# Optimization experiments

Measured on AMD Instinct MI355X. Metric: run time of the kernel, lower is better.

## Reference

```python
import jax, jax.numpy as jnp
import numpy as np

B, N, C, H = 128, 8732, 512, 19  # batch, priors, channels, feature map side
IMG = 300.0
FG = 19


def setup_inputs() -> dict:
    key = jax.random.key(0)
    ks = jax.random.split(key, 10)
    loc = jax.random.normal(ks[0], (B, N, 4), jnp.float32) * 0.5
    conf = jax.random.normal(ks[1], (B, N, 2), jnp.float32)
    priors = jax.random.uniform(ks[2], (N, 4), jnp.float32, minval=0.05, maxval=0.95)
    features = jax.random.normal(ks[3], (B, C, H, H), jnp.float32)
    w1 = jax.random.normal(ks[4], (C, 4096), jnp.float32) * 0.01
    b1 = jnp.zeros((4096,), jnp.float32)
    w2 = jax.random.normal(ks[5], (4096, 4096), jnp.float32) * 0.01
    b2 = jnp.zeros((4096,), jnp.float32)
    w3 = jax.random.normal(ks[6], (4096, FG), jnp.float32) * 0.01
    b3 = jnp.zeros((FG,), jnp.float32)
    return {"loc": loc, "conf": conf, "priors": priors, "features": features,
            "w1": w1, "b1": b1, "w2": w2, "b2": b2, "w3": w3, "b3": b3}


def _decode(loc, priors):
    # SSD decode, variances=[0.1, 0.2]; priors are (cx, cy, w, h)
    cxcy = priors[:, :2] + loc[..., :2] * 0.1 * priors[:, 2:]
    wh = priors[:, 2:] * jnp.exp(loc[..., 2:] * 0.2)
    xy1 = cxcy - 0.5 * wh
    return jnp.concatenate([xy1, xy1 + wh], axis=-1)  # [B,N,4] corner form


def _best_prior(loc, conf, priors):
    boxes = _decode(loc, priors)                       # [B,N,4]
    probs = jax.nn.softmax(conf, axis=-1)              # [B,N,2]
    car = jnp.argmax(probs, axis=-1) == 1              # [B,N] argmax class == car
    score = jnp.where(car, probs[..., 1], -jnp.inf)
    best = jnp.argmax(score, axis=-1)                  # [B]
    best_box = jnp.take_along_axis(boxes, best[:, None, None], axis=1)[:, 0]  # [B,4]
    has_car = jnp.any(car, axis=-1)                    # [B]
    geom = (best_box[:, 2] > best_box[:, 0]) & (best_box[:, 3] > best_box[:, 1])
    valid = has_car & geom
    result = jnp.where(has_car[:, None], best_box, 0.0)
    result = jnp.clip(result, 0.0, 1.0)
    return result, valid


def _extract(features, boxes, valid):
    # per-box crop + global max pool -> [B,C], zero for invalid boxes
    ceil_num = features.shape[2]
    step = IMG / ceil_num
    b = jnp.clip(boxes * IMG, 0.0, IMG) / step
    b = jnp.floor(jnp.clip(b, 0.0, ceil_num - 1.0)).astype(jnp.int32)  # [B,4]=x1,y1,x2,y2
    r = jnp.arange(ceil_num)
    mh = (r[None, :] >= b[:, 1:2]) & (r[None, :] <= b[:, 3:4])  # [B,H] rows
    mw = (r[None, :] >= b[:, 0:1]) & (r[None, :] <= b[:, 2:3])  # [B,W] cols
    mask = mh[:, None, :, None] & mw[:, None, None, :]          # [B,1,H,W]
    m = jnp.max(jnp.where(mask, features, -jnp.inf), axis=(2, 3))  # [B,C]
    return jnp.where(valid[:, None], m, 0.0)


def reference(loc, conf, priors, features, w1, b1, w2, b2, w3, b3):
    boxes, valid = _best_prior(loc, conf, priors)
    feat = _extract(features, boxes, valid)             # [B,512]
    h = jax.nn.relu(feat @ w1 + b1)
    h = jax.nn.relu(h @ w2 + b2)
    fg_cls = h @ w3 + b3                                # [B,19]
    return fg_cls, boxes, valid.astype(jnp.int32)
```

## Files before the change

kernel.cpp:

```cpp
#include <hip/hip_runtime.h>
#include <hip/hip_bf16.h>
#include <math.h>

#define BATCH 128
#define NPRI  8732
#define CCH   512
#define HH    19
#define NHID  4096
#define FGC   19

typedef unsigned short u16;
typedef __attribute__((ext_vector_type(8))) short bf16x8;
typedef __attribute__((ext_vector_type(4))) float f32x4;

__device__ __forceinline__ u16 f2bf(float f) {
  unsigned u = __float_as_uint(f);
  u += 0x7fff + ((u >> 16) & 1);
  return (u16)(u >> 16);
}

__global__ void k_best_partial(const float* __restrict__ conf,
                               float* __restrict__ cs, int* __restrict__ ci,
                               int* __restrict__ cc) {
  int blk = blockIdx.x;
  int b = blk >> 2, chunk = blk & 3;
  int n0 = chunk * 2183;
  int t = threadIdx.x;
  const float* cb = conf + (size_t)b * NPRI * 2;
  float bestS = -INFINITY; int bestN = 0x7fffffff; int car_any = 0;
  for (int i = n0 + t; i < n0 + 2183; i += 256) {
    float c0 = cb[2 * i], c1 = cb[2 * i + 1];
    float m = fmaxf(c0, c1);
    float e0 = expf(c0 - m), e1 = expf(c1 - m);
    float s = e0 + e1;
    float p0 = e0 / s, p1 = e1 / s;
    bool car = p1 > p0;
    car_any |= (int)car;
    float sc = car ? p1 : -INFINITY;
    if (sc > bestS || (sc == bestS && i < bestN)) { bestS = sc; bestN = i; }
  }
  __shared__ float ls[256]; __shared__ int li[256]; __shared__ int lc[256];
  ls[t] = bestS; li[t] = bestN; lc[t] = car_any;
  __syncthreads();
  for (int off = 128; off > 0; off >>= 1) {
    if (t < off) {
      float s2 = ls[t + off]; int n2 = li[t + off];
      if (s2 > ls[t] || (s2 == ls[t] && n2 < li[t])) { ls[t] = s2; li[t] = n2; }
      lc[t] |= lc[t + off];
    }
    __syncthreads();
  }
  if (t == 0) { cs[blk] = ls[0]; ci[blk] = li[0]; cc[blk] = lc[0]; }
}

__global__ void k_best_final(const float* __restrict__ loc,
                             const float* __restrict__ priors,
                             const float* __restrict__ cs,
                             const int* __restrict__ ci,
                             const int* __restrict__ cc,
                             float* __restrict__ out_boxes,
                             float* __restrict__ out_valid,
                             int4* __restrict__ crop,
                             int* __restrict__ vflag) {
  int b = threadIdx.x;
  if (b >= BATCH) return;
  float bs = -INFINITY; int bn = 0; int hc = 0;
  #pragma unroll
  for (int p = 0; p < 4; p++) {
    float s = cs[b * 4 + p]; int n = ci[b * 4 + p];
    hc |= cc[b * 4 + p];
    if (s > bs) { bs = s; bn = n; }
  }
  const float* lp = loc + ((size_t)b * NPRI + bn) * 4;
  const float* pp = priors + (size_t)bn * 4;
  float l0 = lp[0], l1 = lp[1], l2 = lp[2], l3 = lp[3];
  float pcx = pp[0], pcy = pp[1], pw = pp[2], ph = pp[3];
  float cx = pcx + (l0 * 0.1f) * pw;
  float cy = pcy + (l1 * 0.1f) * ph;
  float w = pw * expf(l2 * 0.2f);
  float h = ph * expf(l3 * 0.2f);
  float x1 = cx - 0.5f * w;
  float y1 = cy - 0.5f * h;
  float x2 = x1 + w, y2 = y1 + h;
  bool geom = (x2 > x1) && (y2 > y1);
  bool valid = hc && geom;
  float r0, r1, r2, r3;
  if (hc) { r0 = x1; r1 = y1; r2 = x2; r3 = y2; }
  else    { r0 = r1 = r2 = r3 = 0.0f; }
  r0 = fminf(fmaxf(r0, 0.0f), 1.0f);
  r1 = fminf(fmaxf(r1, 0.0f), 1.0f);
  r2 = fminf(fmaxf(r2, 0.0f), 1.0f);
  r3 = fminf(fmaxf(r3, 0.0f), 1.0f);
  out_boxes[b * 4 + 0] = r0; out_boxes[b * 4 + 1] = r1;
  out_boxes[b * 4 + 2] = r2; out_boxes[b * 4 + 3] = r3;
  out_valid[b] = valid ? 1.0f : 0.0f;
  const float stepF = (float)(300.0 / 19.0);
  float q0 = fminf(fmaxf(r0 * 300.0f, 0.0f), 300.0f) / stepF;
  float q1 = fminf(fmaxf(r1 * 300.0f, 0.0f), 300.0f) / stepF;
  float q2 = fminf(fmaxf(r2 * 300.0f, 0.0f), 300.0f) / stepF;
  float q3 = fminf(fmaxf(r3 * 300.0f, 0.0f), 300.0f) / stepF;
  int ix1 = (int)floorf(fminf(fmaxf(q0, 0.0f), 18.0f));
  int iy1 = (int)floorf(fminf(fmaxf(q1, 0.0f), 18.0f));
  int ix2 = (int)floorf(fminf(fmaxf(q2, 0.0f), 18.0f));
  int iy2 = (int)floorf(fminf(fmaxf(q3, 0.0f), 18.0f));
  crop[b] = make_int4(ix1, iy1, ix2, iy2);
  vflag[b] = valid ? 1 : 0;
}

__global__ void k_extract(const float* __restrict__ fin,
                          const int4* __restrict__ crop,
                          const int* __restrict__ vflag,
                          u16* __restrict__ feat) {
  int blk = blockIdx.x;
  int b = blk >> 7;
  int tile = blk & 127;
  int wave = threadIdx.x >> 6;
  int lane = threadIdx.x & 63;
  int c = tile * 4 + wave;
  if (!vflag[b]) {
    if (lane == 0) feat[b * CCH + c] = 0;
    return;
  }
  int4 cr = crop[b];
  int wcnt = cr.z - cr.x + 1;
  int cnt = wcnt * (cr.w - cr.y + 1);
  const float* p = fin + (size_t)(b * CCH + c) * (HH * HH);
  float m = -INFINITY;
  for (int i = lane; i < cnt; i += 64) {
    int yy = cr.y + i / wcnt;
    int xx = cr.x + i % wcnt;
    m = fmaxf(m, p[yy * HH + xx]);
  }
  #pragma unroll
  for (int off = 32; off > 0; off >>= 1) m = fmaxf(m, __shfl_xor(m, off));
  if (lane == 0) feat[b * CCH + c] = f2bf(m);
}

template <int KSPL>
__global__ __launch_bounds__(256) void k_mfma(const u16* __restrict__ A,
                                              const float* __restrict__ W,
                                              float* __restrict__ part, int K) {
  const int N = 4096;
  const int BK = 32;
  int nb = blockIdx.x;
  int ks = blockIdx.y;
  int Kper = K / KSPL;
  int k0b = ks * Kper;
  int t = threadIdx.x;
  int lane = t & 63, wave = t >> 6;
  int q = lane >> 4, r = lane & 15;

  __shared__ u16 As[128 * 40];
  __shared__ u16 Bs[64 * 40];

  int wm = (wave & 1) * 64;
  int wn = (wave >> 1) * 32;
  int n0 = nb * 64;

  f32x4 acc[4][2];
  #pragma unroll
  for (int i = 0; i < 4; i++)
    #pragma unroll
    for (int j = 0; j < 2; j++) {
      acc[i][j].x = 0.f; acc[i][j].y = 0.f; acc[i][j].z = 0.f; acc[i][j].w = 0.f;
    }

  int am = t >> 1, ah = (t & 1) * 16;
  int kp = t >> 4;
  int n4 = (t & 15) * 4;

  for (int k0 = k0b; k0 < k0b + Kper; k0 += BK) {
    const u16* asrc = A + (size_t)am * K + k0 + ah;
    uint4 a0 = *(const uint4*)asrc;
    uint4 a1 = *(const uint4*)(asrc + 8);
    const float* wsrc = W + (size_t)(k0 + 2 * kp) * N + n0 + n4;
    float4 w0 = *(const float4*)wsrc;
    float4 w1 = *(const float4*)(wsrc + N);
    __syncthreads();
    *(uint4*)&As[am * 40 + ah]     = a0;
    *(uint4*)&As[am * 40 + ah + 8] = a1;
    {
      unsigned pk0 = (unsigned)f2bf(w0.x) | ((unsigned)f2bf(w1.x) << 16);
      unsigned pk1 = (unsigned)f2bf(w0.y) | ((unsigned)f2bf(w1.y) << 16);
      unsigned pk2 = (unsigned)f2bf(w0.z) | ((unsigned)f2bf(w1.z) << 16);
      unsigned pk3 = (unsigned)f2bf(w0.w) | ((unsigned)f2bf(w1.w) << 16);
      *(unsigned*)&Bs[(n4 + 0) * 40 + 2 * kp] = pk0;
      *(unsigned*)&Bs[(n4 + 1) * 40 + 2 * kp] = pk1;
      *(unsigned*)&Bs[(n4 + 2) * 40 + 2 * kp] = pk2;
      *(unsigned*)&Bs[(n4 + 3) * 40 + 2 * kp] = pk3;
    }
    __syncthreads();
    bf16x8 af[4], bfr[2];
    #pragma unroll
    for (int i = 0; i < 4; i++)
      af[i] = *(const bf16x8*)&As[(wm + 16 * i + r) * 40 + q * 8];
    #pragma unroll
    for (int j = 0; j < 2; j++)
      bfr[j] = *(const bf16x8*)&Bs[(wn + 16 * j + r) * 40 + q * 8];
    #pragma unroll
    for (int i = 0; i < 4; i++)
      #pragma unroll
      for (int j = 0; j < 2; j++)
        acc[i][j] = __builtin_amdgcn_mfma_f32_16x16x32_bf16(af[i], bfr[j],
                                                            acc[i][j], 0, 0, 0);
  }

  float* dst = part + (size_t)ks * (BATCH * N);
  #pragma unroll
  for (int i = 0; i < 4; i++)
    #pragma unroll
    for (int j = 0; j < 2; j++) {
      int col = n0 + wn + 16 * j + r;
      #pragma unroll
      for (int reg = 0; reg < 4; reg++) {
        int row = wm + 16 * i + q * 4 + reg;
        dst[(size_t)row * N + col] = acc[i][j][reg];
      }
    }
}

template <int KSPL, bool BF16OUT>
__global__ void k_finalize(const float* __restrict__ part,
                           const float* __restrict__ bias,
                           float* __restrict__ outf,
                           u16* __restrict__ outb) {
  int idx = (blockIdx.x * 256 + threadIdx.x) * 4;
  float4 s = *(const float4*)(part + idx);
  #pragma unroll
  for (int p = 1; p < KSPL; p++) {
    float4 v = *(const float4*)(part + (size_t)p * (BATCH * NHID) + idx);
    s.x += v.x; s.y += v.y; s.z += v.z; s.w += v.w;
  }
  float4 bv = *(const float4*)(bias + (idx & (NHID - 1)));
  s.x = fmaxf(s.x + bv.x, 0.0f); s.y = fmaxf(s.y + bv.y, 0.0f);
  s.z = fmaxf(s.z + bv.z, 0.0f); s.w = fmaxf(s.w + bv.w, 0.0f);
  if (BF16OUT) {
    ushort4 o;
    o.x = f2bf(s.x); o.y = f2bf(s.y); o.z = f2bf(s.z); o.w = f2bf(s.w);
    *(ushort4*)(outb + idx) = o;
  } else {
    *(float4*)(outf + idx) = s;
  }
}

__global__ void k_gemm3p(const float* __restrict__ h2,
                         const float* __restrict__ w3,
                         float* __restrict__ part3) {
  int kc = blockIdx.x;
  int t = threadIdx.x;
  __shared__ float wl[32 * FGC];
  for (int i = t; i < 32 * FGC; i += 128) wl[i] = w3[kc * 32 * FGC + i];
  __syncthreads();
  const float* hp = h2 + (size_t)t * NHID + kc * 32;
  float acc[FGC];
  #pragma unroll
  for (int j = 0; j < FGC; j++) acc[j] = 0.0f;
  for (int k = 0; k < 32; k++) {
    float hv = hp[k];
    const float* wp = &wl[k * FGC];
    #pragma unroll
    for (int j = 0; j < FGC; j++) acc[j] += hv * wp[j];
  }
  float* dst = part3 + (size_t)kc * (BATCH * FGC) + t * FGC;
  #pragma unroll
  for (int j = 0; j < FGC; j++) dst[j] = acc[j];
}

__global__ void k_fin3(const float* __restrict__ part3,
                       const float* __restrict__ b3,
                       float* __restrict__ out) {
  int j = blockIdx.x * 256 + threadIdx.x;
  if (j >= BATCH * FGC) return;
  float s = 0.0f;
  for (int p = 0; p < 128; p++) s += part3[(size_t)p * (BATCH * FGC) + j];
  out[j] = s + b3[j % FGC];
}

extern "C" void kernel_launch(void* const* d_in, const int* in_sizes, int n_in,
                              void* d_out, int out_size, void* d_ws, size_t ws_size,
                              hipStream_t stream) {
  const float* loc      = (const float*)d_in[0];
  const float* conf     = (const float*)d_in[1];
  const float* priors   = (const float*)d_in[2];
  const float* features = (const float*)d_in[3];
  const float* w1 = (const float*)d_in[4];
  const float* b1 = (const float*)d_in[5];
  const float* w2 = (const float*)d_in[6];
  const float* b2 = (const float*)d_in[7];
  const float* w3 = (const float*)d_in[8];
  const float* b3 = (const float*)d_in[9];
  float* out = (float*)d_out;

  char* ws = (char*)d_ws;
  float* part  = (float*)ws;
  float* part3 = (float*)(ws + (size_t)16 * 1024 * 1024);
  float* h2    = (float*)(ws + (size_t)18 * 1024 * 1024);
  u16*   featb = (u16*)(ws + (size_t)20 * 1024 * 1024);
  u16*   h1b   = (u16*)(ws + (size_t)20 * 1024 * 1024 + 256 * 1024);
  float* cs    = (float*)(ws + (size_t)21 * 1024 * 1024);
  int*   ci    = (int*)(cs + 512);
  int*   cc    = ci + 512;
  int4*  crop  = (int4*)(cc + 512);
  int*   vfl   = (int*)(crop + BATCH);

  k_best_partial<<<512, 256, 0, stream>>>(conf, cs, ci, cc);
  k_best_final<<<1, 128, 0, stream>>>(loc, priors, cs, ci, cc,
                                      out + BATCH * FGC,
                                      out + BATCH * FGC + BATCH * 4, crop, vfl);
  k_extract<<<BATCH * (CCH / 4), 256, 0, stream>>>(features, crop, vfl, featb);
  k_mfma<4><<<dim3(64, 4), 256, 0, stream>>>(featb, w1, part, 512);
  k_finalize<4, true><<<512, 256, 0, stream>>>(part, b1, nullptr, h1b);
  k_mfma<8><<<dim3(64, 8), 256, 0, stream>>>(h1b, w2, part, 4096);
  k_finalize<8, false><<<512, 256, 0, stream>>>(part, b2, h2, nullptr);
  k_gemm3p<<<128, 128, 0, stream>>>(h2, w3, part3);
  k_fin3<<<10, 256, 0, stream>>>(part3, b3, out);
}
```

Measured before the change: 260.6 us.

## Fuse whole pipeline into one cooperative persistent kernel with grid syncs

Replaces nine separate kernel launches with one cooperative kernel of 512 blocks that runs every stage in sequence, separated by grid-wide barriers. The best-prior search now uses one block per batch row and compares logit differences instead of computing softmax. The first GEMM now uses a K split of 8 instead of 4, and the final 19-wide projection becomes one block per row with shuffle reductions. The aim is to remove per-launch overhead and intermediate round trips, at the cost of grid-sync latency and fewer blocks in the extract and final-projection stages.

```diff
diff --git a/kernel.cpp b/kernel.cpp
--- a/kernel.cpp
+++ b/kernel.cpp
@@ -1,6 +1,8 @@
 #include <hip/hip_runtime.h>
-#include <hip/hip_bf16.h>
+#include <hip/hip_cooperative_groups.h>
 #include <math.h>
+
+namespace cg = cooperative_groups;
 
 #define BATCH 128
 #define NPRI  8732
@@ -8,6 +10,8 @@
 #define HH    19
 #define NHID  4096
 #define FGC   19
+#define GRID  512
+#define KSPL  8
 
 typedef unsigned short u16;
 typedef __attribute__((ext_vector_type(8))) short bf16x8;
@@ -19,142 +23,25 @@
   return (u16)(u >> 16);
 }
 
-__global__ void k_best_partial(const float* __restrict__ conf,
-                               float* __restrict__ cs, int* __restrict__ ci,
-                               int* __restrict__ cc) {
-  int blk = blockIdx.x;
-  int b = blk >> 2, chunk = blk & 3;
-  int n0 = chunk * 2183;
-  int t = threadIdx.x;
-  const float* cb = conf + (size_t)b * NPRI * 2;
-  float bestS = -INFINITY; int bestN = 0x7fffffff; int car_any = 0;
-  for (int i = n0 + t; i < n0 + 2183; i += 256) {
-    float c0 = cb[2 * i], c1 = cb[2 * i + 1];
-    float m = fmaxf(c0, c1);
-    float e0 = expf(c0 - m), e1 = expf(c1 - m);
-    float s = e0 + e1;
-    float p0 = e0 / s, p1 = e1 / s;
-    bool car = p1 > p0;
-    car_any |= (int)car;
-    float sc = car ? p1 : -INFINITY;
-    if (sc > bestS || (sc == bestS && i < bestN)) { bestS = sc; bestN = i; }
-  }
-  __shared__ float ls[256]; __shared__ int li[256]; __shared__ int lc[256];
-  ls[t] = bestS; li[t] = bestN; lc[t] = car_any;
-  __syncthreads();
-  for (int off = 128; off > 0; off >>= 1) {
-    if (t < off) {
-      float s2 = ls[t + off]; int n2 = li[t + off];
-      if (s2 > ls[t] || (s2 == ls[t] && n2 < li[t])) { ls[t] = s2; li[t] = n2; }
-      lc[t] |= lc[t + off];
-    }
-    __syncthreads();
-  }
-  if (t == 0) { cs[blk] = ls[0]; ci[blk] = li[0]; cc[blk] = lc[0]; }
-}
-
-__global__ void k_best_final(const float* __restrict__ loc,
-                             const float* __restrict__ priors,
-                             const float* __restrict__ cs,
-                             const int* __restrict__ ci,
-                             const int* __restrict__ cc,
-                             float* __restrict__ out_boxes,
-                             float* __restrict__ out_valid,
-                             int4* __restrict__ crop,
-                             int* __restrict__ vflag) {
-  int b = threadIdx.x;
-  if (b >= BATCH) return;
-  float bs = -INFINITY; int bn = 0; int hc = 0;
-  #pragma unroll
-  for (int p = 0; p < 4; p++) {
-    float s = cs[b * 4 + p]; int n = ci[b * 4 + p];
-    hc |= cc[b * 4 + p];
-    if (s > bs) { bs = s; bn = n; }
-  }
-  const float* lp = loc + ((size_t)b * NPRI + bn) * 4;
-  const float* pp = priors + (size_t)bn * 4;
-  float l0 = lp[0], l1 = lp[1], l2 = lp[2], l3 = lp[3];
-  float pcx = pp[0], pcy = pp[1], pw = pp[2], ph = pp[3];
-  float cx = pcx + (l0 * 0.1f) * pw;
-  float cy = pcy + (l1 * 0.1f) * ph;
-  float w = pw * expf(l2 * 0.2f);
-  float h = ph * expf(l3 * 0.2f);
-  float x1 = cx - 0.5f * w;
-  float y1 = cy - 0.5f * h;
-  float x2 = x1 + w, y2 = y1 + h;
-  bool geom = (x2 > x1) && (y2 > y1);
-  bool valid = hc && geom;
-  float r0, r1, r2, r3;
-  if (hc) { r0 = x1; r1 = y1; r2 = x2; r3 = y2; }
-  else    { r0 = r1 = r2 = r3 = 0.0f; }
-  r0 = fminf(fmaxf(r0, 0.0f), 1.0f);
-  r1 = fminf(fmaxf(r1, 0.0f), 1.0f);
-  r2 = fminf(fmaxf(r2, 0.0f), 1.0f);
-  r3 = fminf(fmaxf(r3, 0.0f), 1.0f);
-  out_boxes[b * 4 + 0] = r0; out_boxes[b * 4 + 1] = r1;
-  out_boxes[b * 4 + 2] = r2; out_boxes[b * 4 + 3] = r3;
-  out_valid[b] = valid ? 1.0f : 0.0f;
-  const float stepF = (float)(300.0 / 19.0);
-  float q0 = fminf(fmaxf(r0 * 300.0f, 0.0f), 300.0f) / stepF;
-  float q1 = fminf(fmaxf(r1 * 300.0f, 0.0f), 300.0f) / stepF;
-  float q2 = fminf(fmaxf(r2 * 300.0f, 0.0f), 300.0f) / stepF;
-  float q3 = fminf(fmaxf(r3 * 300.0f, 0.0f), 300.0f) / stepF;
-  int ix1 = (int)floorf(fminf(fmaxf(q0, 0.0f), 18.0f));
-  int iy1 = (int)floorf(fminf(fmaxf(q1, 0.0f), 18.0f));
-  int ix2 = (int)floorf(fminf(fmaxf(q2, 0.0f), 18.0f));
-  int iy2 = (int)floorf(fminf(fmaxf(q3, 0.0f), 18.0f));
-  crop[b] = make_int4(ix1, iy1, ix2, iy2);
-  vflag[b] = valid ? 1 : 0;
-}
-
-__global__ void k_extract(const float* __restrict__ fin,
-                          const int4* __restrict__ crop,
-                          const int* __restrict__ vflag,
-                          u16* __restrict__ feat) {
-  int blk = blockIdx.x;
-  int b = blk >> 7;
-  int tile = blk & 127;
-  int wave = threadIdx.x >> 6;
-  int lane = threadIdx.x & 63;
-  int c = tile * 4 + wave;
-  if (!vflag[b]) {
-    if (lane == 0) feat[b * CCH + c] = 0;
-    return;
-  }
-  int4 cr = crop[b];
-  int wcnt = cr.z - cr.x + 1;
-  int cnt = wcnt * (cr.w - cr.y + 1);
-  const float* p = fin + (size_t)(b * CCH + c) * (HH * HH);
-  float m = -INFINITY;
-  for (int i = lane; i < cnt; i += 64) {
-    int yy = cr.y + i / wcnt;
-    int xx = cr.x + i % wcnt;
-    m = fmaxf(m, p[yy * HH + xx]);
-  }
-  #pragma unroll
-  for (int off = 32; off > 0; off >>= 1) m = fmaxf(m, __shfl_xor(m, off));
-  if (lane == 0) feat[b * CCH + c] = f2bf(m);
-}
-
-template <int KSPL>
-__global__ __launch_bounds__(256) void k_mfma(const u16* __restrict__ A,
-                                              const float* __restrict__ W,
-                                              float* __restrict__ part, int K) {
-  const int N = 4096;
-  const int BK = 32;
-  int nb = blockIdx.x;
-  int ks = blockIdx.y;
-  int Kper = K / KSPL;
+struct SMem {
+  union {
+    struct { float s[256]; int n[256]; } red;
+    struct { u16 As[128 * 40]; u16 Bs[64 * 40]; } mm;
+    float g3[4 * FGC];
+  };
+};
+
+__device__ void mfma_phase(const u16* __restrict__ A, const float* __restrict__ W,
+                           float* __restrict__ part, int K, int Kper,
+                           u16* As, u16* Bs) {
+  const int N = NHID;
+  int bid = blockIdx.x;
+  int nb = bid & 63, ks = bid >> 6;
   int k0b = ks * Kper;
   int t = threadIdx.x;
   int lane = t & 63, wave = t >> 6;
   int q = lane >> 4, r = lane & 15;
-
-  __shared__ u16 As[128 * 40];
-  __shared__ u16 Bs[64 * 40];
-
-  int wm = (wave & 1) * 64;
-  int wn = (wave >> 1) * 32;
+  int wm = (wave & 1) * 64, wn = (wave >> 1) * 32;
   int n0 = nb * 64;
 
   f32x4 acc[4][2];
@@ -169,21 +56,21 @@
   int kp = t >> 4;
   int n4 = (t & 15) * 4;
 
-  for (int k0 = k0b; k0 < k0b + Kper; k0 += BK) {
+  for (int k0 = k0b; k0 < k0b + Kper; k0 += 32) {
     const u16* asrc = A + (size_t)am * K + k0 + ah;
     uint4 a0 = *(const uint4*)asrc;
     uint4 a1 = *(const uint4*)(asrc + 8);
     const float* wsrc = W + (size_t)(k0 + 2 * kp) * N + n0 + n4;
     float4 w0 = *(const float4*)wsrc;
-    float4 w1 = *(const float4*)(wsrc + N);
+    float4 w1v = *(const float4*)(wsrc + N);
     __syncthreads();
     *(uint4*)&As[am * 40 + ah]     = a0;
     *(uint4*)&As[am * 40 + ah + 8] = a1;
     {
-      unsigned pk0 = (unsigned)f2bf(w0.x) | ((unsigned)f2bf(w1.x) << 16);
-      unsigned pk1 = (unsigned)f2bf(w0.y) | ((unsigned)f2bf(w1.y) << 16);
-      unsigned pk2 = (unsigned)f2bf(w0.z) | ((unsigned)f2bf(w1.z) << 16);
-      unsigned pk3 = (unsigned)f2bf(w0.w) | ((unsigned)f2bf(w1.w) << 16);
+      unsigned pk0 = (unsigned)f2bf(w0.x) | ((unsigned)f2bf(w1v.x) << 16);
+      unsigned pk1 = (unsigned)f2bf(w0.y) | ((unsigned)f2bf(w1v.y) << 16);
+      unsigned pk2 = (unsigned)f2bf(w0.z) | ((unsigned)f2bf(w1v.z) << 16);
+      unsigned pk3 = (unsigned)f2bf(w0.w) | ((unsigned)f2bf(w1v.w) << 16);
       *(unsigned*)&Bs[(n4 + 0) * 40 + 2 * kp] = pk0;
       *(unsigned*)&Bs[(n4 + 1) * 40 + 2 * kp] = pk1;
       *(unsigned*)&Bs[(n4 + 2) * 40 + 2 * kp] = pk2;
@@ -205,7 +92,7 @@
                                                             acc[i][j], 0, 0, 0);
   }
 
-  float* dst = part + (size_t)ks * (BATCH * N);
+  float* dst = part + (size_t)ks * (BATCH * NHID);
   #pragma unroll
   for (int i = 0; i < 4; i++)
     #pragma unroll
@@ -219,61 +106,171 @@
     }
 }
 
-template <int KSPL, bool BF16OUT>
-__global__ void k_finalize(const float* __restrict__ part,
-                           const float* __restrict__ bias,
-                           float* __restrict__ outf,
-                           u16* __restrict__ outb) {
-  int idx = (blockIdx.x * 256 + threadIdx.x) * 4;
-  float4 s = *(const float4*)(part + idx);
-  #pragma unroll
-  for (int p = 1; p < KSPL; p++) {
-    float4 v = *(const float4*)(part + (size_t)p * (BATCH * NHID) + idx);
-    s.x += v.x; s.y += v.y; s.z += v.z; s.w += v.w;
-  }
-  float4 bv = *(const float4*)(bias + (idx & (NHID - 1)));
-  s.x = fmaxf(s.x + bv.x, 0.0f); s.y = fmaxf(s.y + bv.y, 0.0f);
-  s.z = fmaxf(s.z + bv.z, 0.0f); s.w = fmaxf(s.w + bv.w, 0.0f);
-  if (BF16OUT) {
+__global__ __launch_bounds__(256, 2) void fused_net(
+    const float* __restrict__ loc, const float* __restrict__ conf,
+    const float* __restrict__ priors, const float* __restrict__ features,
+    const float* __restrict__ w1, const float* __restrict__ b1,
+    const float* __restrict__ w2, const float* __restrict__ b2,
+    const float* __restrict__ w3, const float* __restrict__ b3,
+    float* __restrict__ out, float* __restrict__ part,
+    u16* __restrict__ featb, u16* __restrict__ h1b, float* __restrict__ h2,
+    int4* __restrict__ crop, int* __restrict__ vfl) {
+  __shared__ __align__(16) SMem sm;
+  cg::grid_group grid = cg::this_grid();
+  int t = threadIdx.x;
+
+  if (blockIdx.x < BATCH) {
+    int b = blockIdx.x;
+    const float4* cb = (const float4*)(conf + (size_t)b * NPRI * 2);
+    float bd = -INFINITY; int bn = 0x7fffffff;
+    for (int j = t; j < NPRI / 2; j += 256) {
+      float4 v = cb[j];
+      float d0 = v.y - v.x, d1 = v.w - v.z;
+      if (d0 > bd) { bd = d0; bn = 2 * j; }
+      if (d1 > bd) { bd = d1; bn = 2 * j + 1; }
+    }
+    sm.red.s[t] = bd; sm.red.n[t] = bn;
+    __syncthreads();
+    for (int off = 128; off > 0; off >>= 1) {
+      if (t < off) {
+        float s2 = sm.red.s[t + off]; int n2 = sm.red.n[t + off];
+        if (s2 > sm.red.s[t] || (s2 == sm.red.s[t] && n2 < sm.red.n[t])) {
+          sm.red.s[t] = s2; sm.red.n[t] = n2;
+        }
+      }
+      __syncthreads();
+    }
+    if (t == 0) {
+      float bdf = sm.red.s[0]; int bnf = sm.red.n[0];
+      bool hc = bdf > 0.0f;
+      float r0 = 0.f, r1 = 0.f, r2 = 0.f, r3 = 0.f;
+      bool valid = false;
+      if (hc) {
+        const float* lp = loc + ((size_t)b * NPRI + bnf) * 4;
+        const float* pp = priors + (size_t)bnf * 4;
+        float l0 = lp[0], l1 = lp[1], l2 = lp[2], l3 = lp[3];
+        float pcx = pp[0], pcy = pp[1], pw = pp[2], ph = pp[3];
+        float cx = pcx + (l0 * 0.1f) * pw;
+        float cy = pcy + (l1 * 0.1f) * ph;
+        float w = pw * expf(l2 * 0.2f);
+        float h = ph * expf(l3 * 0.2f);
+        float x1 = cx - 0.5f * w, y1 = cy - 0.5f * h;
+        float x2 = x1 + w, y2 = y1 + h;
+        valid = (x2 > x1) && (y2 > y1);
+        r0 = fminf(fmaxf(x1, 0.f), 1.f);
+        r1 = fminf(fmaxf(y1, 0.f), 1.f);
+        r2 = fminf(fmaxf(x2, 0.f), 1.f);
+        r3 = fminf(fmaxf(y2, 0.f), 1.f);
+      }
+      float* ob = out + BATCH * FGC;
+      ob[b * 4 + 0] = r0; ob[b * 4 + 1] = r1;
+      ob[b * 4 + 2] = r2; ob[b * 4 + 3] = r3;
+      out[BATCH * FGC + BATCH * 4 + b] = valid ? 1.0f : 0.0f;
+      const float stepF = (float)(300.0 / 19.0);
+      float q0 = fminf(fmaxf(r0 * 300.0f, 0.0f), 300.0f) / stepF;
+      float q1 = fminf(fmaxf(r1 * 300.0f, 0.0f), 300.0f) / stepF;
+      float q2 = fminf(fmaxf(r2 * 300.0f, 0.0f), 300.0f) / stepF;
+      float q3 = fminf(fmaxf(r3 * 300.0f, 0.0f), 300.0f) / stepF;
+      int ix1 = (int)floorf(fminf(fmaxf(q0, 0.0f), 18.0f));
+      int iy1 = (int)floorf(fminf(fmaxf(q1, 0.0f), 18.0f));
+      int ix2 = (int)floorf(fminf(fmaxf(q2, 0.0f), 18.0f));
+      int iy2 = (int)floorf(fminf(fmaxf(q3, 0.0f), 18.0f));
+      crop[b] = make_int4(ix1, iy1, ix2, iy2);
+      vfl[b] = valid ? 1 : 0;
+    }
+  }
+  grid.sync();
+
+  {
+    int wave = t >> 6, lane = t & 63;
+    for (int v = blockIdx.x; v < BATCH * (CCH / 4); v += GRID) {
+      int b = v >> 7, tile = v & 127;
+      int c = tile * 4 + wave;
+      if (!vfl[b]) { if (lane == 0) featb[b * CCH + c] = 0; continue; }
+      int4 cr = crop[b];
+      int wcnt = cr.z - cr.x + 1;
+      int cnt = wcnt * (cr.w - cr.y + 1);
+      const float* p = features + (size_t)(b * CCH + c) * (HH * HH);
+      float m = -INFINITY;
+      for (int i = lane; i < cnt; i += 64) {
+        int yy = cr.y + i / wcnt;
+        int xx = cr.x + i % wcnt;
+        m = fmaxf(m, p[yy * HH + xx]);
+      }
+      #pragma unroll
+      for (int off = 32; off > 0; off >>= 1) m = fmaxf(m, __shfl_xor(m, off));
+      if (lane == 0) featb[b * CCH + c] = f2bf(m);
+    }
+  }
+  grid.sync();
+
+  mfma_phase(featb, w1, part, CCH, CCH / KSPL, sm.mm.As, sm.mm.Bs);
+  grid.sync();
+
+  {
+    int idx = (blockIdx.x * 256 + t) * 4;
+    float4 s = *(const float4*)(part + idx);
+    #pragma unroll
+    for (int p = 1; p < KSPL; p++) {
+      float4 v = *(const float4*)(part + (size_t)p * (BATCH * NHID) + idx);
+      s.x += v.x; s.y += v.y; s.z += v.z; s.w += v.w;
+    }
+    float4 bv = *(const float4*)(b1 + (idx & (NHID - 1)));
+    s.x = fmaxf(s.x + bv.x, 0.0f); s.y = fmaxf(s.y + bv.y, 0.0f);
+    s.z = fmaxf(s.z + bv.z, 0.0f); s.w = fmaxf(s.w + bv.w, 0.0f);
     ushort4 o;
     o.x = f2bf(s.x); o.y = f2bf(s.y); o.z = f2bf(s.z); o.w = f2bf(s.w);
-    *(ushort4*)(outb + idx) = o;
-  } else {
-    *(float4*)(outf + idx) = s;
-  }
-}
-
-__global__ void k_gemm3p(const float* __restrict__ h2,
-                         const float* __restrict__ w3,
-                         float* __restrict__ part3) {
-  int kc = blockIdx.x;
-  int t = threadIdx.x;
-  __shared__ float wl[32 * FGC];
-  for (int i = t; i < 32 * FGC; i += 128) wl[i] = w3[kc * 32 * FGC + i];
-  __syncthreads();
-  const float* hp = h2 + (size_t)t * NHID + kc * 32;
-  float acc[FGC];
-  #pragma unroll
-  for (int j = 0; j < FGC; j++) acc[j] = 0.0f;
-  for (int k = 0; k < 32; k++) {
-    float hv = hp[k];
-    const float* wp = &wl[k * FGC];
-    #pragma unroll
-    for (int j = 0; j < FGC; j++) acc[j] += hv * wp[j];
-  }
-  float* dst = part3 + (size_t)kc * (BATCH * FGC) + t * FGC;
-  #pragma unroll
-  for (int j = 0; j < FGC; j++) dst[j] = acc[j];
-}
-
-__global__ void k_fin3(const float* __restrict__ part3,
-                       const float* __restrict__ b3,
-                       float* __restrict__ out) {
-  int j = blockIdx.x * 256 + threadIdx.x;
-  if (j >= BATCH * FGC) return;
-  float s = 0.0f;
-  for (int p = 0; p < 128; p++) s += part3[(size_t)p * (BATCH * FGC) + j];
-  out[j] = s + b3[j % FGC];
+    *(ushort4*)(h1b + idx) = o;
+  }
+  grid.sync();
+
+  mfma_phase(h1b, w2, part, NHID, NHID / KSPL, sm.mm.As, sm.mm.Bs);
+  grid.sync();
+
+  {
+    int idx = (blockIdx.x * 256 + t) * 4;
+    float4 s = *(const float4*)(part + idx);
+    #pragma unroll
+    for (int p = 1; p < KSPL; p++) {
+      float4 v = *(const float4*)(part + (size_t)p * (BATCH * NHID) + idx);
+      s.x += v.x; s.y += v.y; s.z += v.z; s.w += v.w;
+    }
+    float4 bv = *(const float4*)(b2 + (idx & (NHID - 1)));
+    s.x = fmaxf(s.x + bv.x, 0.0f); s.y = fmaxf(s.y + bv.y, 0.0f);
+    s.z = fmaxf(s.z + bv.z, 0.0f); s.w = fmaxf(s.w + bv.w, 0.0f);
+    *(float4*)(h2 + idx) = s;
+  }
+  grid.sync();
+
+  if (blockIdx.x < BATCH) {
+    int b = blockIdx.x;
+    float acc[FGC];
+    #pragma unroll
+    for (int j = 0; j < FGC; j++) acc[j] = 0.0f;
+    const float* hp = h2 + (size_t)b * NHID;
+    for (int k = t; k < NHID; k += 256) {
+      float hv = hp[k];
+      const float* wp = w3 + (size_t)k * FGC;
+      #pragma unroll
+      for (int j = 0; j < FGC; j++) acc[j] += hv * wp[j];
+    }
+    int lane = t & 63, wave = t >> 6;
+    #pragma unroll
+    for (int j = 0; j < FGC; j++) {
+      #pragma unroll
+      for (int off = 32; off > 0; off >>= 1)
+        acc[j] += __shfl_xor(acc[j], off);
+    }
+    if (lane == 0) {
+      #pragma unroll
+      for (int j = 0; j < FGC; j++) sm.g3[wave * FGC + j] = acc[j];
+    }
+    __syncthreads();
+    if (t < FGC) {
+      float s = sm.g3[t] + sm.g3[FGC + t] + sm.g3[2 * FGC + t] + sm.g3[3 * FGC + t];
+      out[b * FGC + t] = s + b3[t];
+    }
+  }
 }
 
 extern "C" void kernel_launch(void* const* d_in, const int* in_sizes, int n_in,
@@ -293,25 +290,18 @@
 
   char* ws = (char*)d_ws;
   float* part  = (float*)ws;
-  float* part3 = (float*)(ws + (size_t)16 * 1024 * 1024);
+  u16*   featb = (u16*)(ws + (size_t)16 * 1024 * 1024);
+  u16*   h1b   = (u16*)(ws + (size_t)16 * 1024 * 1024 + 256 * 1024);
   float* h2    = (float*)(ws + (size_t)18 * 1024 * 1024);
-  u16*   featb = (u16*)(ws + (size_t)20 * 1024 * 1024);
-  u16*   h1b   = (u16*)(ws + (size_t)20 * 1024 * 1024 + 256 * 1024);
-  float* cs    = (float*)(ws + (size_t)21 * 1024 * 1024);
-  int*   ci    = (int*)(cs + 512);
-  int*   cc    = ci + 512;
-  int4*  crop  = (int4*)(cc + 512);
+  int4*  crop  = (int4*)(ws + (size_t)20 * 1024 * 1024);
   int*   vfl   = (int*)(crop + BATCH);
 
-  k_best_partial<<<512, 256, 0, stream>>>(conf, cs, ci, cc);
-  k_best_final<<<1, 128, 0, stream>>>(loc, priors, cs, ci, cc,
-                                      out + BATCH * FGC,
-                                      out + BATCH * FGC + BATCH * 4, crop, vfl);
-  k_extract<<<BATCH * (CCH / 4), 256, 0, stream>>>(features, crop, vfl, featb);
-  k_mfma<4><<<dim3(64, 4), 256, 0, stream>>>(featb, w1, part, 512);
-  k_finalize<4, true><<<512, 256, 0, stream>>>(part, b1, nullptr, h1b);
-  k_mfma<8><<<dim3(64, 8), 256, 0, stream>>>(h1b, w2, part, 4096);
-  k_finalize<8, false><<<512, 256, 0, stream>>>(part, b2, h2, nullptr);
-  k_gemm3p<<<128, 128, 0, stream>>>(h2, w3, part3);
-  k_fin3<<<10, 256, 0, stream>>>(part3, b3, out);
+  void* args[] = {
+    (void*)&loc, (void*)&conf, (void*)&priors, (void*)&features,
+    (void*)&w1, (void*)&b1, (void*)&w2, (void*)&b2, (void*)&w3, (void*)&b3,
+    (void*)&out, (void*)&part, (void*)&featb, (void*)&h1b, (void*)&h2,
+    (void*)&crop, (void*)&vfl
+  };
+  hipLaunchCooperativeKernel((void*)fused_net, dim3(GRID), dim3(256),
+                             args, 0, stream);
 }
```

After: 650.2 us. 150% more time.

## Fuse best-prior search into one kernel, fuse GEMM1 bias/ReLU, branchless crop max

Applied to the files above, without the earlier changes.

The best-prior stage becomes one kernel per batch row. It reads conf as float4 and compares logit differences instead of computing softmax, and the same kernel decodes the chosen box. GEMM1 now runs without a K split and applies bias, ReLU and bf16 conversion in its epilogue, which removes the partial-sum buffer and a finalize launch. The crop max-pool reads the whole 19x19 map with a fixed unrolled loop and masks out pixels outside the box, replacing per-element div/mod. The trade-off is fewer blocks for GEMM1 (64) and more loads in extract.

```diff
diff --git a/kernel.cpp b/kernel.cpp
--- a/kernel.cpp
+++ b/kernel.cpp
@@ -1,5 +1,4 @@
 #include <hip/hip_runtime.h>
-#include <hip/hip_bf16.h>
 #include <math.h>
 
 #define BATCH 128
@@ -19,92 +18,69 @@
   return (u16)(u >> 16);
 }
 
-__global__ void k_best_partial(const float* __restrict__ conf,
-                               float* __restrict__ cs, int* __restrict__ ci,
-                               int* __restrict__ cc) {
-  int blk = blockIdx.x;
-  int b = blk >> 2, chunk = blk & 3;
-  int n0 = chunk * 2183;
+__global__ void k_best(const float* __restrict__ conf,
+                       const float* __restrict__ loc,
+                       const float* __restrict__ priors,
+                       float* __restrict__ out_boxes,
+                       float* __restrict__ out_valid,
+                       int4* __restrict__ crop, int* __restrict__ vflag) {
+  int b = blockIdx.x;
   int t = threadIdx.x;
-  const float* cb = conf + (size_t)b * NPRI * 2;
-  float bestS = -INFINITY; int bestN = 0x7fffffff; int car_any = 0;
-  for (int i = n0 + t; i < n0 + 2183; i += 256) {
-    float c0 = cb[2 * i], c1 = cb[2 * i + 1];
-    float m = fmaxf(c0, c1);
-    float e0 = expf(c0 - m), e1 = expf(c1 - m);
-    float s = e0 + e1;
-    float p0 = e0 / s, p1 = e1 / s;
-    bool car = p1 > p0;
-    car_any |= (int)car;
-    float sc = car ? p1 : -INFINITY;
-    if (sc > bestS || (sc == bestS && i < bestN)) { bestS = sc; bestN = i; }
-  }
-  __shared__ float ls[256]; __shared__ int li[256]; __shared__ int lc[256];
-  ls[t] = bestS; li[t] = bestN; lc[t] = car_any;
+  const float4* cb = (const float4*)(conf + (size_t)b * NPRI * 2);
+  float bd = -INFINITY; int bn = 0x7fffffff;
+  for (int j = t; j < NPRI / 2; j += 256) {
+    float4 v = cb[j];
+    float d0 = v.y - v.x, d1 = v.w - v.z;
+    if (d0 > bd) { bd = d0; bn = 2 * j; }
+    if (d1 > bd) { bd = d1; bn = 2 * j + 1; }
+  }
+  __shared__ float ls[256]; __shared__ int li[256];
+  ls[t] = bd; li[t] = bn;
   __syncthreads();
   for (int off = 128; off > 0; off >>= 1) {
     if (t < off) {
       float s2 = ls[t + off]; int n2 = li[t + off];
       if (s2 > ls[t] || (s2 == ls[t] && n2 < li[t])) { ls[t] = s2; li[t] = n2; }
-      lc[t] |= lc[t + off];
-    }
-    __syncthreads();
-  }
-  if (t == 0) { cs[blk] = ls[0]; ci[blk] = li[0]; cc[blk] = lc[0]; }
-}
-
-__global__ void k_best_final(const float* __restrict__ loc,
-                             const float* __restrict__ priors,
-                             const float* __restrict__ cs,
-                             const int* __restrict__ ci,
-                             const int* __restrict__ cc,
-                             float* __restrict__ out_boxes,
-                             float* __restrict__ out_valid,
-                             int4* __restrict__ crop,
-                             int* __restrict__ vflag) {
-  int b = threadIdx.x;
-  if (b >= BATCH) return;
-  float bs = -INFINITY; int bn = 0; int hc = 0;
-  #pragma unroll
-  for (int p = 0; p < 4; p++) {
-    float s = cs[b * 4 + p]; int n = ci[b * 4 + p];
-    hc |= cc[b * 4 + p];
-    if (s > bs) { bs = s; bn = n; }
-  }
-  const float* lp = loc + ((size_t)b * NPRI + bn) * 4;
-  const float* pp = priors + (size_t)bn * 4;
-  float l0 = lp[0], l1 = lp[1], l2 = lp[2], l3 = lp[3];
-  float pcx = pp[0], pcy = pp[1], pw = pp[2], ph = pp[3];
-  float cx = pcx + (l0 * 0.1f) * pw;
-  float cy = pcy + (l1 * 0.1f) * ph;
-  float w = pw * expf(l2 * 0.2f);
-  float h = ph * expf(l3 * 0.2f);
-  float x1 = cx - 0.5f * w;
-  float y1 = cy - 0.5f * h;
-  float x2 = x1 + w, y2 = y1 + h;
-  bool geom = (x2 > x1) && (y2 > y1);
-  bool valid = hc && geom;
-  float r0, r1, r2, r3;
-  if (hc) { r0 = x1; r1 = y1; r2 = x2; r3 = y2; }
-  else    { r0 = r1 = r2 = r3 = 0.0f; }
-  r0 = fminf(fmaxf(r0, 0.0f), 1.0f);
-  r1 = fminf(fmaxf(r1, 0.0f), 1.0f);
-  r2 = fminf(fmaxf(r2, 0.0f), 1.0f);
-  r3 = fminf(fmaxf(r3, 0.0f), 1.0f);
-  out_boxes[b * 4 + 0] = r0; out_boxes[b * 4 + 1] = r1;
-  out_boxes[b * 4 + 2] = r2; out_boxes[b * 4 + 3] = r3;
-  out_valid[b] = valid ? 1.0f : 0.0f;
-  const float stepF = (float)(300.0 / 19.0);
-  float q0 = fminf(fmaxf(r0 * 300.0f, 0.0f), 300.0f) / stepF;
-  float q1 = fminf(fmaxf(r1 * 300.0f, 0.0f), 300.0f) / stepF;
-  float q2 = fminf(fmaxf(r2 * 300.0f, 0.0f), 300.0f) / stepF;
-  float q3 = fminf(fmaxf(r3 * 300.0f, 0.0f), 300.0f) / stepF;
-  int ix1 = (int)floorf(fminf(fmaxf(q0, 0.0f), 18.0f));
-  int iy1 = (int)floorf(fminf(fmaxf(q1, 0.0f), 18.0f));
-  int ix2 = (int)floorf(fminf(fmaxf(q2, 0.0f), 18.0f));
-  int iy2 = (int)floorf(fminf(fmaxf(q3, 0.0f), 18.0f));
-  crop[b] = make_int4(ix1, iy1, ix2, iy2);
-  vflag[b] = valid ? 1 : 0;
+    }
+    __syncthreads();
+  }
+  if (t == 0) {
+    float bdf = ls[0]; int bnf = li[0];
+    bool hc = bdf > 0.0f;
+    float r0 = 0.f, r1 = 0.f, r2 = 0.f, r3 = 0.f;
+    bool valid = false;
+    if (hc) {
+      const float* lp = loc + ((size_t)b * NPRI + bnf) * 4;
+      const float* pp = priors + (size_t)bnf * 4;
+      float l0 = lp[0], l1 = lp[1], l2 = lp[2], l3 = lp[3];
+      float pcx = pp[0], pcy = pp[1], pw = pp[2], ph = pp[3];
+      float cx = pcx + (l0 * 0.1f) * pw;
+      float cy = pcy + (l1 * 0.1f) * ph;
+      float w = pw * expf(l2 * 0.2f);
+      float h = ph * expf(l3 * 0.2f);
+      float x1 = cx - 0.5f * w, y1 = cy - 0.5f * h;
+      float x2 = x1 + w, y2 = y1 + h;
+      valid = (x2 > x1) && (y2 > y1);
+      r0 = fminf(fmaxf(x1, 0.f), 1.f);
+      r1 = fminf(fmaxf(y1, 0.f), 1.f);
+      r2 = fminf(fmaxf(x2, 0.f), 1.f);
+      r3 = fminf(fmaxf(y2, 0.f), 1.f);
+    }
+    out_boxes[b * 4 + 0] = r0; out_boxes[b * 4 + 1] = r1;
+    out_boxes[b * 4 + 2] = r2; out_boxes[b * 4 + 3] = r3;
+    out_valid[b] = valid ? 1.0f : 0.0f;
+    const float stepF = (float)(300.0 / 19.0);
+    float q0 = fminf(fmaxf(r0 * 300.0f, 0.0f), 300.0f) / stepF;
+    float q1 = fminf(fmaxf(r1 * 300.0f, 0.0f), 300.0f) / stepF;
+    float q2 = fminf(fmaxf(r2 * 300.0f, 0.0f), 300.0f) / stepF;
+    float q3 = fminf(fmaxf(r3 * 300.0f, 0.0f), 300.0f) / stepF;
+    int ix1 = (int)floorf(fminf(fmaxf(q0, 0.0f), 18.0f));
+    int iy1 = (int)floorf(fminf(fmaxf(q1, 0.0f), 18.0f));
+    int ix2 = (int)floorf(fminf(fmaxf(q2, 0.0f), 18.0f));
+    int iy2 = (int)floorf(fminf(fmaxf(q3, 0.0f), 18.0f));
+    crop[b] = make_int4(ix1, iy1, ix2, iy2);
+    vflag[b] = valid ? 1 : 0;
+  }
 }
 
 __global__ void k_extract(const float* __restrict__ fin,
@@ -122,26 +98,107 @@
     return;
   }
   int4 cr = crop[b];
-  int wcnt = cr.z - cr.x + 1;
-  int cnt = wcnt * (cr.w - cr.y + 1);
   const float* p = fin + (size_t)(b * CCH + c) * (HH * HH);
   float m = -INFINITY;
-  for (int i = lane; i < cnt; i += 64) {
-    int yy = cr.y + i / wcnt;
-    int xx = cr.x + i % wcnt;
-    m = fmaxf(m, p[yy * HH + xx]);
+  #pragma unroll
+  for (int it = 0; it < 6; it++) {
+    int idx = it * 64 + lane;
+    if (idx < HH * HH) {
+      int yy = idx / HH, xx = idx - yy * HH;
+      bool in = (yy >= cr.y) & (yy <= cr.w) & (xx >= cr.x) & (xx <= cr.z);
+      float v = p[idx];
+      if (in) m = fmaxf(m, v);
+    }
   }
   #pragma unroll
   for (int off = 32; off > 0; off >>= 1) m = fmaxf(m, __shfl_xor(m, off));
   if (lane == 0) feat[b * CCH + c] = f2bf(m);
+}
+
+__global__ __launch_bounds__(256) void k_gemm1(const u16* __restrict__ A,
+                                               const float* __restrict__ W,
+                                               const float* __restrict__ bias,
+                                               u16* __restrict__ H1) {
+  const int N = NHID, K = CCH;
+  int nb = blockIdx.x;
+  int t = threadIdx.x;
+  int lane = t & 63, wave = t >> 6;
+  int q = lane >> 4, r = lane & 15;
+  int wm = (wave & 1) * 64, wn = (wave >> 1) * 32;
+  int n0 = nb * 64;
+
+  __shared__ u16 As[128 * 40];
+  __shared__ u16 Bs[64 * 40];
+
+  f32x4 acc[4][2];
+  #pragma unroll
+  for (int i = 0; i < 4; i++)
+    #pragma unroll
+    for (int j = 0; j < 2; j++) {
+      acc[i][j].x = 0.f; acc[i][j].y = 0.f; acc[i][j].z = 0.f; acc[i][j].w = 0.f;
+    }
+
+  int am = t >> 1, ah = (t & 1) * 16;
+  int kp = t >> 4;
+  int n4 = (t & 15) * 4;
+
+  for (int k0 = 0; k0 < K; k0 += 32) {
+    const u16* asrc = A + (size_t)am * K + k0 + ah;
+    uint4 a0 = *(const uint4*)asrc;
+    uint4 a1 = *(const uint4*)(asrc + 8);
+    const float* wsrc = W + (size_t)(k0 + 2 * kp) * N + n0 + n4;
+    float4 w0 = *(const float4*)wsrc;
+    float4 w1v = *(const float4*)(wsrc + N);
+    __syncthreads();
+    *(uint4*)&As[am * 40 + ah]     = a0;
+    *(uint4*)&As[am * 40 + ah + 8] = a1;
+    {
+      unsigned pk0 = (unsigned)f2bf(w0.x) | ((unsigned)f2bf(w1v.x) << 16);
+      unsigned pk1 = (unsigned)f2bf(w0.y) | ((unsigned)f2bf(w1v.y) << 16);
+      unsigned pk2 = (unsigned)f2bf(w0.z) | ((unsigned)f2bf(w1v.z) << 16);
+      unsigned pk3 = (unsigned)f2bf(w0.w) | ((unsigned)f2bf(w1v.w) << 16);
+      *(unsigned*)&Bs[(n4 + 0) * 40 + 2 * kp] = pk0;
+      *(unsigned*)&Bs[(n4 + 1) * 40 + 2 * kp] = pk1;
+      *(unsigned*)&Bs[(n4 + 2) * 40 + 2 * kp] = pk2;
+      *(unsigned*)&Bs[(n4 + 3) * 40 + 2 * kp] = pk3;
+    }
+    __syncthreads();
+    bf16x8 af[4], bfr[2];
+    #pragma unroll
+    for (int i = 0; i < 4; i++)
+      af[i] = *(const bf16x8*)&As[(wm + 16 * i + r) * 40 + q * 8];
+    #pragma unroll
+    for (int j = 0; j < 2; j++)
+      bfr[j] = *(const bf16x8*)&Bs[(wn + 16 * j + r) * 40 + q * 8];
+    #pragma unroll
+    for (int i = 0; i < 4; i++)
+      #pragma unroll
+      for (int j = 0; j < 2; j++)
+        acc[i][j] = __builtin_amdgcn_mfma_f32_16x16x32_bf16(af[i], bfr[j],
+                                                            acc[i][j], 0, 0, 0);
+  }
+
+  #pragma unroll
+  for (int j = 0; j < 2; j++) {
+    int col = n0 + wn + 16 * j + r;
+    float bv = bias[col];
+    #pragma unroll
+    for (int i = 0; i < 4; i++) {
+      #pragma unroll
+      for (int reg = 0; reg < 4; reg++) {
+        int row = wm + 16 * i + q * 4 + reg;
+        float v = fmaxf(acc[i][j][reg] + bv, 0.0f);
+        H1[(size_t)row * N + col] = f2bf(v);
+      }
+    }
+  }
 }
 
 template <int KSPL>
 __global__ __launch_bounds__(256) void k_mfma(const u16* __restrict__ A,
                                               const float* __restrict__ W,
                                               float* __restrict__ part, int K) {
-  const int N = 4096;
-  const int BK = 32;
+  const int N = NHID;
   int nb = blockIdx.x;
   int ks = blockIdx.y;
   int Kper = K / KSPL;
@@ -169,21 +226,21 @@
   int kp = t >> 4;
   int n4 = (t & 15) * 4;
 
-  for (int k0 = k0b; k0 < k0b + Kper; k0 += BK) {
+  for (int k0 = k0b; k0 < k0b + Kper; k0 += 32) {
     const u16* asrc = A + (size_t)am * K + k0 + ah;
     uint4 a0 = *(const uint4*)asrc;
     uint4 a1 = *(const uint4*)(asrc + 8);
     const float* wsrc = W + (size_t)(k0 + 2 * kp) * N + n0 + n4;
     float4 w0 = *(const float4*)wsrc;
-    float4 w1 = *(const float4*)(wsrc + N);
+    float4 w1v = *(const float4*)(wsrc + N);
     __syncthreads();
     *(uint4*)&As[am * 40 + ah]     = a0;
     *(uint4*)&As[am * 40 + ah + 8] = a1;
     {
-      unsigned pk0 = (unsigned)f2bf(w0.x) | ((unsigned)f2bf(w1.x) << 16);
-      unsigned pk1 = (unsigned)f2bf(w0.y) | ((unsigned)f2bf(w1.y) << 16);
-      unsigned pk2 = (unsigned)f2bf(w0.z) | ((unsigned)f2bf(w1.z) << 16);
-      unsigned pk3 = (unsigned)f2bf(w0.w) | ((unsigned)f2bf(w1.w) << 16);
+      unsigned pk0 = (unsigned)f2bf(w0.x) | ((unsigned)f2bf(w1v.x) << 16);
+      unsigned pk1 = (unsigned)f2bf(w0.y) | ((unsigned)f2bf(w1v.y) << 16);
+      unsigned pk2 = (unsigned)f2bf(w0.z) | ((unsigned)f2bf(w1v.z) << 16);
+      unsigned pk3 = (unsigned)f2bf(w0.w) | ((unsigned)f2bf(w1v.w) << 16);
       *(unsigned*)&Bs[(n4 + 0) * 40 + 2 * kp] = pk0;
       *(unsigned*)&Bs[(n4 + 1) * 40 + 2 * kp] = pk1;
       *(unsigned*)&Bs[(n4 + 2) * 40 + 2 * kp] = pk2;
@@ -205,7 +262,7 @@
                                                             acc[i][j], 0, 0, 0);
   }
 
-  float* dst = part + (size_t)ks * (BATCH * N);
+  float* dst = part + (size_t)ks * (BATCH * NHID);
   #pragma unroll
   for (int i = 0; i < 4; i++)
     #pragma unroll
@@ -219,11 +276,10 @@
     }
 }
 
-template <int KSPL, bool BF16OUT>
+template <int KSPL>
 __global__ void k_finalize(const float* __restrict__ part,
                            const float* __restrict__ bias,
-                           float* __restrict__ outf,
-                           u16* __restrict__ outb) {
+                           float* __restrict__ outf) {
   int idx = (blockIdx.x * 256 + threadIdx.x) * 4;
   float4 s = *(const float4*)(part + idx);
   #pragma unroll
@@ -234,13 +290,7 @@
   float4 bv = *(const float4*)(bias + (idx & (NHID - 1)));
   s.x = fmaxf(s.x + bv.x, 0.0f); s.y = fmaxf(s.y + bv.y, 0.0f);
   s.z = fmaxf(s.z + bv.z, 0.0f); s.w = fmaxf(s.w + bv.w, 0.0f);
-  if (BF16OUT) {
-    ushort4 o;
-    o.x = f2bf(s.x); o.y = f2bf(s.y); o.z = f2bf(s.z); o.w = f2bf(s.w);
-    *(ushort4*)(outb + idx) = o;
-  } else {
-    *(float4*)(outf + idx) = s;
-  }
+  *(float4*)(outf + idx) = s;
 }
 
 __global__ void k_gemm3p(const float* __restrict__ h2,
@@ -297,21 +347,16 @@
   float* h2    = (float*)(ws + (size_t)18 * 1024 * 1024);
   u16*   featb = (u16*)(ws + (size_t)20 * 1024 * 1024);
   u16*   h1b   = (u16*)(ws + (size_t)20 * 1024 * 1024 + 256 * 1024);
-  float* cs    = (float*)(ws + (size_t)21 * 1024 * 1024);
-  int*   ci    = (int*)(cs + 512);
-  int*   cc    = ci + 512;
-  int4*  crop  = (int4*)(cc + 512);
+  int4*  crop  = (int4*)(ws + (size_t)21 * 1024 * 1024 + 512 * 1024);
   int*   vfl   = (int*)(crop + BATCH);
 
-  k_best_partial<<<512, 256, 0, stream>>>(conf, cs, ci, cc);
-  k_best_final<<<1, 128, 0, stream>>>(loc, priors, cs, ci, cc,
-                                      out + BATCH * FGC,
-                                      out + BATCH * FGC + BATCH * 4, crop, vfl);
+  k_best<<<BATCH, 256, 0, stream>>>(conf, loc, priors,
+                                    out + BATCH * FGC,
+                                    out + BATCH * FGC + BATCH * 4, crop, vfl);
   k_extract<<<BATCH * (CCH / 4), 256, 0, stream>>>(features, crop, vfl, featb);
-  k_mfma<4><<<dim3(64, 4), 256, 0, stream>>>(featb, w1, part, 512);
-  k_finalize<4, true><<<512, 256, 0, stream>>>(part, b1, nullptr, h1b);
-  k_mfma<8><<<dim3(64, 8), 256, 0, stream>>>(h1b, w2, part, 4096);
-  k_finalize<8, false><<<512, 256, 0, stream>>>(part, b2, h2, nullptr);
+  k_gemm1<<<64, 256, 0, stream>>>(featb, w1, b1, h1b);
+  k_mfma<8><<<dim3(64, 8), 256, 0, stream>>>(h1b, w2, part, NHID);
+  k_finalize<8><<<512, 256, 0, stream>>>(part, b2, h2);
   k_gemm3p<<<128, 128, 0, stream>>>(h2, w3, part3);
   k_fin3<<<10, 256, 0, stream>>>(part3, b3, out);
 }
```

Measured after the change: 275.1 us. 5.6% more time.
